# Kernel tuning notes

Measured on AMD Instinct MI355X. Metric: run time of the kernel, lower is better.

The kernel has to match this reference:

```python
import jax, jax.numpy as jnp
import numpy as np
import math

B, N = 8, 131072
IN_C, OUT_C, STYLE_DIM, K = 64, 64, 256, 1
EPS = 1e-08


def setup_inputs() -> dict:
    key = jax.random.key(0)
    k1, k2, k3, k4 = jax.random.split(key, 4)
    x = jax.random.normal(k1, (B, N, IN_C), dtype=jnp.float32)
    style = jax.random.normal(k2, (B, STYLE_DIM), dtype=jnp.float32)
    # main conv weight: torch stores (1, out_c, in_c, k, k); k=1 -> (out_c, in_c)
    weight = jax.random.normal(k3, (OUT_C, IN_C), dtype=jnp.float32)
    bias = jnp.zeros((OUT_C,), dtype=jnp.float32)
    # EqualLinear modulation: weight (in_c, style_dim), bias init 0 -> style*scale+0, then +1
    mod_weight = jax.random.normal(k4, (IN_C, STYLE_DIM), dtype=jnp.float32)
    mod_bias = jnp.zeros((IN_C,), dtype=jnp.float32)
    return {"x": x, "style": style, "weight": weight, "bias": bias,
            "mod_weight": mod_weight, "mod_bias": mod_bias}


def reference(x, style, weight, bias, mod_weight, mod_bias):
    scale = 1.0 / math.sqrt(IN_C * K * K)          # conv weight scale
    mod_scale = 1.0 / math.sqrt(STYLE_DIM)         # EqualLinear scale (lr_mul=1)
    # modulation: EqualLinear(style) + 1  -> (b, in_c)
    s = style @ (mod_weight * mod_scale).T + mod_bias + 1.0
    # per-sample modulated weight: (b, out_c, in_c)
    w = scale * weight[None, :, :] * s[:, None, :]
    # demodulate over (in_c, k, k); k=1 so just in_c
    demod = jax.lax.rsqrt(jnp.sum(w * w, axis=2) + EPS)  # (b, out_c)
    w = w * demod[:, :, None]
    # grouped 1x1 conv == per-sample matmul over points: (b, n, out_c)
    out = jnp.einsum('bni,boi->bno', x, w) + bias[None, None, :]
    return out
```

## Files before the change

kernel.cpp:

```cpp
#include <hip/hip_runtime.h>
#include <hip/hip_bf16.h>

#define B_  8
#define N_  131072
#define C_  64
#define SD_ 256

typedef __attribute__((ext_vector_type(8))) short  short8;
typedef __attribute__((ext_vector_type(4))) float  floatx4;

static __device__ inline short bf16_of(float f) {
    __hip_bfloat16 h = __float2bfloat16(f);
    return *reinterpret_cast<short*>(&h);
}

__global__ void modw_kernel(const float* __restrict__ style,
                            const float* __restrict__ weight,
                            const float* __restrict__ mod_weight,
                            const float* __restrict__ mod_bias,
                            __hip_bfloat16* __restrict__ wout) {
    const int b = blockIdx.x;
    const int t = threadIdx.x;
    __shared__ float part[4][64];
    __shared__ float s_sh[64];

    const int i   = t & 63;
    const int seg = t >> 6;
    {
        const float* st = style + b * SD_ + seg * 64;
        const float* mw = mod_weight + i * SD_ + seg * 64;
        float p = 0.f;
        #pragma unroll
        for (int d = 0; d < 64; ++d) p += st[d] * mw[d];
        part[seg][i] = p;
    }
    __syncthreads();
    if (t < 64) {
        float s = (part[0][t] + part[1][t] + part[2][t] + part[3][t]) * 0.0625f
                  + mod_bias[t] + 1.0f;
        s_sh[t] = s;
    }
    __syncthreads();
    if (t < 64) {
        const int o = t;
        float wt[64];
        float sumsq = 0.f;
        #pragma unroll
        for (int ii = 0; ii < 64; ++ii) {
            float v = 0.125f * weight[o * 64 + ii] * s_sh[ii];
            wt[ii] = v;
            sumsq += v * v;
        }
        const float demod = rsqrtf(sumsq + 1e-8f);
        #pragma unroll
        for (int ii = 0; ii < 64; ++ii)
            wout[(b * 64 + o) * 64 + ii] = __float2bfloat16(wt[ii] * demod);
    }
}

__global__ __launch_bounds__(256) void conv_kernel(
        const float* __restrict__ x,
        const __hip_bfloat16* __restrict__ wmod,
        const float* __restrict__ bias,
        float* __restrict__ out) {
    const int lane = threadIdx.x & 63;
    const int wid  = threadIdx.x >> 6;
    const int gw   = blockIdx.x * 4 + wid;
    const int b    = gw >> 11;
    const int p0   = (gw & 2047) * 64;
    const int row  = lane & 15;
    const int quad = lane >> 4;

    short8 wf[4][2];
    const short* wb = (const short*)(wmod) + b * 64 * 64;
    #pragma unroll
    for (int mt = 0; mt < 4; ++mt)
        #pragma unroll
        for (int ks = 0; ks < 2; ++ks)
            wf[mt][ks] = *(const short8*)(wb + (mt * 16 + row) * 64 + ks * 32 + quad * 8);

    floatx4 bias_v[4];
    #pragma unroll
    for (int mt = 0; mt < 4; ++mt)
        bias_v[mt] = *(const floatx4*)(bias + mt * 16 + quad * 4);

    const size_t base = ((size_t)b * N_ + p0) * C_;
    const float* xb = x + base;
    float*       ob = out + base;

    #pragma unroll
    for (int pt = 0; pt < 4; ++pt) {
        const float* xr = xb + (pt * 16 + row) * C_ + quad * 8;
        floatx4 a0 = *(const floatx4*)(xr);
        floatx4 a1 = *(const floatx4*)(xr + 4);
        floatx4 a2 = *(const floatx4*)(xr + 32);
        floatx4 a3 = *(const floatx4*)(xr + 36);

        short8 xf0, xf1;
        #pragma unroll
        for (int j = 0; j < 4; ++j) {
            xf0[j]     = bf16_of(a0[j]);
            xf0[j + 4] = bf16_of(a1[j]);
            xf1[j]     = bf16_of(a2[j]);
            xf1[j + 4] = bf16_of(a3[j]);
        }

        floatx4 acc[4];
        #pragma unroll
        for (int mt = 0; mt < 4; ++mt) {
            acc[mt] = bias_v[mt];
            acc[mt] = __builtin_amdgcn_mfma_f32_16x16x32_bf16(wf[mt][0], xf0, acc[mt], 0, 0, 0);
            acc[mt] = __builtin_amdgcn_mfma_f32_16x16x32_bf16(wf[mt][1], xf1, acc[mt], 0, 0, 0);
        }

        float* orow = ob + (pt * 16 + row) * C_ + quad * 4;
        #pragma unroll
        for (int mt = 0; mt < 4; ++mt)
            __builtin_nontemporal_store(acc[mt], (floatx4*)(orow + mt * 16));
    }
}

extern "C" void kernel_launch(void* const* d_in, const int* in_sizes, int n_in,
                              void* d_out, int out_size, void* d_ws, size_t ws_size,
                              hipStream_t stream) {
    const float* x          = (const float*)d_in[0];
    const float* style      = (const float*)d_in[1];
    const float* weight     = (const float*)d_in[2];
    const float* bias       = (const float*)d_in[3];
    const float* mod_weight = (const float*)d_in[4];
    const float* mod_bias   = (const float*)d_in[5];
    float* out = (float*)d_out;
    __hip_bfloat16* wmod = (__hip_bfloat16*)d_ws;

    modw_kernel<<<dim3(B_), dim3(256), 0, stream>>>(style, weight, mod_weight, mod_bias, wmod);
    conv_kernel<<<dim3((B_ * N_) / 256), dim3(256), 0, stream>>>(x, wmod, bias, out);
}
```

Baseline: 470.4 us.

## Stage x tiles through LDS via global_load_lds and coalesce output stores

Each wave now bulk-loads its 64x64 fp32 x tile straight into LDS with global_load_lds, issuing all loads up front. MFMA fragments are read from LDS, and results are written back into the same LDS region and then stored to global memory as fully contiguous 16-byte-per-lane rows. Before this, each lane did strided row loads and stores. The aim is more memory-level parallelism and better-coalesced global traffic in this bandwidth-bound kernel. The costs are 64KB of LDS per block, which limits occupancy, and the loss of nontemporal stores. The in-place LDS reuse also relies on wave-local ordering with no explicit barrier.

```diff
diff --git a/kernel.cpp b/kernel.cpp
--- a/kernel.cpp
+++ b/kernel.cpp
@@ -8,6 +8,9 @@
 
 typedef __attribute__((ext_vector_type(8))) short  short8;
 typedef __attribute__((ext_vector_type(4))) float  floatx4;
+
+typedef const __attribute__((address_space(1))) void  cglb_t;
+typedef       __attribute__((address_space(3))) void  lds_t;
 
 static __device__ inline short bf16_of(float f) {
     __hip_bfloat16 h = __float2bfloat16(f);
@@ -58,7 +61,7 @@
     }
 }
 
-__global__ __launch_bounds__(256) void conv_kernel(
+__global__ __launch_bounds__(256, 4) void conv_kernel(
         const float* __restrict__ x,
         const __hip_bfloat16* __restrict__ wmod,
         const float* __restrict__ bias,
@@ -71,30 +74,48 @@
     const int row  = lane & 15;
     const int quad = lane >> 4;
 
-    short8 wf[4][2];
-    const short* wb = (const short*)(wmod) + b * 64 * 64;
-    #pragma unroll
-    for (int mt = 0; mt < 4; ++mt)
-        #pragma unroll
-        for (int ks = 0; ks < 2; ++ks)
-            wf[mt][ks] = *(const short8*)(wb + (mt * 16 + row) * 64 + ks * 32 + quad * 8);
-
-    floatx4 bias_v[4];
-    #pragma unroll
-    for (int mt = 0; mt < 4; ++mt)
-        bias_v[mt] = *(const floatx4*)(bias + mt * 16 + quad * 4);
+    __shared__ __align__(16) float smem[4 * 4096];
+    float* ws = smem + wid * 4096;
 
     const size_t base = ((size_t)b * N_ + p0) * C_;
     const float* xb = x + base;
     float*       ob = out + base;
 
     #pragma unroll
-    for (int pt = 0; pt < 4; ++pt) {
-        const float* xr = xb + (pt * 16 + row) * C_ + quad * 8;
-        floatx4 a0 = *(const floatx4*)(xr);
-        floatx4 a1 = *(const floatx4*)(xr + 4);
-        floatx4 a2 = *(const floatx4*)(xr + 32);
-        floatx4 a3 = *(const floatx4*)(xr + 36);
+    for (int t = 0; t < 4; ++t)
+        #pragma unroll
+        for (int c = 0; c < 4; ++c)
+            __builtin_amdgcn_global_load_lds(
+                (cglb_t*)(xb + t * 1024 + c * 256 + lane * 4),
+                (lds_t*)(ws + t * 1024 + c * 256),
+                16, 0, 0);
+
+    const short* wb = (const short*)(wmod) + b * 64 * 64;
+    short8 wf00 = *(const short8*)(wb + ( 0 + row) * 64 +  0 + quad * 8);
+    short8 wf01 = *(const short8*)(wb + ( 0 + row) * 64 + 32 + quad * 8);
+    short8 wf10 = *(const short8*)(wb + (16 + row) * 64 +  0 + quad * 8);
+    short8 wf11 = *(const short8*)(wb + (16 + row) * 64 + 32 + quad * 8);
+    short8 wf20 = *(const short8*)(wb + (32 + row) * 64 +  0 + quad * 8);
+    short8 wf21 = *(const short8*)(wb + (32 + row) * 64 + 32 + quad * 8);
+    short8 wf30 = *(const short8*)(wb + (48 + row) * 64 +  0 + quad * 8);
+    short8 wf31 = *(const short8*)(wb + (48 + row) * 64 + 32 + quad * 8);
+
+    floatx4 bias_v0 = *(const floatx4*)(bias +  0 + quad * 4);
+    floatx4 bias_v1 = *(const floatx4*)(bias + 16 + quad * 4);
+    floatx4 bias_v2 = *(const floatx4*)(bias + 32 + quad * 4);
+    floatx4 bias_v3 = *(const floatx4*)(bias + 48 + quad * 4);
+
+    asm volatile("s_waitcnt vmcnt(0)" ::: "memory");
+
+    #pragma unroll
+    for (int t = 0; t < 4; ++t) {
+        float* wt = ws + t * 1024;
+
+        const float* fr = wt + row * 64 + quad * 8;
+        floatx4 a0 = *(const floatx4*)(fr);
+        floatx4 a1 = *(const floatx4*)(fr + 4);
+        floatx4 a2 = *(const floatx4*)(fr + 32);
+        floatx4 a3 = *(const floatx4*)(fr + 36);
 
         short8 xf0, xf1;
         #pragma unroll
@@ -105,18 +126,28 @@
             xf1[j + 4] = bf16_of(a3[j]);
         }
 
-        floatx4 acc[4];
+        floatx4 acc0 = bias_v0, acc1 = bias_v1, acc2 = bias_v2, acc3 = bias_v3;
+        acc0 = __builtin_amdgcn_mfma_f32_16x16x32_bf16(wf00, xf0, acc0, 0, 0, 0);
+        acc0 = __builtin_amdgcn_mfma_f32_16x16x32_bf16(wf01, xf1, acc0, 0, 0, 0);
+        acc1 = __builtin_amdgcn_mfma_f32_16x16x32_bf16(wf10, xf0, acc1, 0, 0, 0);
+        acc1 = __builtin_amdgcn_mfma_f32_16x16x32_bf16(wf11, xf1, acc1, 0, 0, 0);
+        acc2 = __builtin_amdgcn_mfma_f32_16x16x32_bf16(wf20, xf0, acc2, 0, 0, 0);
+        acc2 = __builtin_amdgcn_mfma_f32_16x16x32_bf16(wf21, xf1, acc2, 0, 0, 0);
+        acc3 = __builtin_amdgcn_mfma_f32_16x16x32_bf16(wf30, xf0, acc3, 0, 0, 0);
+        acc3 = __builtin_amdgcn_mfma_f32_16x16x32_bf16(wf31, xf1, acc3, 0, 0, 0);
+
+        float* wo = wt + row * 64 + quad * 4;
+        *(floatx4*)(wo +  0) = acc0;
+        *(floatx4*)(wo + 16) = acc1;
+        *(floatx4*)(wo + 32) = acc2;
+        *(floatx4*)(wo + 48) = acc3;
+
+        float* obt = ob + t * 1024;
         #pragma unroll
-        for (int mt = 0; mt < 4; ++mt) {
-            acc[mt] = bias_v[mt];
-            acc[mt] = __builtin_amdgcn_mfma_f32_16x16x32_bf16(wf[mt][0], xf0, acc[mt], 0, 0, 0);
-            acc[mt] = __builtin_amdgcn_mfma_f32_16x16x32_bf16(wf[mt][1], xf1, acc[mt], 0, 0, 0);
+        for (int c = 0; c < 4; ++c) {
+            floatx4 v = *(const floatx4*)(wt + c * 256 + lane * 4);
+            *(floatx4*)(obt + c * 256 + lane * 4) = v;
         }
-
-        float* orow = ob + (pt * 16 + row) * C_ + quad * 4;
-        #pragma unroll
-        for (int mt = 0; mt < 4; ++mt)
-            __builtin_nontemporal_store(acc[mt], (floatx4*)(orow + mt * 16));
     }
 }
 
```

After: 440.4 us. -6.4%, faster.
